# Optimization experiments

Hardware: AMD Instinct MI355X
Metric: run time of the kernel (lower is better)

The kernel has to match this reference:

```python
import jax, jax.numpy as jnp
import numpy as np

K, N = 4, 128
NODEDIM = 256
EDGEDIM_IN = 256
EDGEDIM_OUT = 256
GLOBALDIM = 256
INFODIM = 2 * NODEDIM + GLOBALDIM + EDGEDIM_IN  # 1024


def setup_inputs() -> dict:
    key = jax.random.key(0)
    ks = jax.random.split(key, 10)
    u = jax.random.normal(ks[0], (K, GLOBALDIM), dtype=jnp.float32)
    h_v = jax.random.normal(ks[1], (K, N, NODEDIM), dtype=jnp.float32)
    h_e = jax.random.normal(ks[2], (K, N, N, EDGEDIM_IN), dtype=jnp.float32)
    V = jax.random.randint(ks[3], (K, N), 0, 2).astype(jnp.float32)  # binary node mask
    E = jax.random.randint(ks[4], (K, N, N, 2), 0, 2, dtype=jnp.int32)  # per-type edge mask
    # function[1] params (loop runs i in [1, num_functions) -> only i=1)
    s1 = 1.0 / np.sqrt(INFODIM)
    W1 = jax.random.uniform(ks[5], (INFODIM, INFODIM), jnp.float32, -s1, s1)
    b1 = jax.random.uniform(ks[6], (INFODIM,), jnp.float32, -s1, s1)
    W2 = jax.random.uniform(ks[7], (INFODIM, EDGEDIM_OUT), jnp.float32, -s1, s1)
    b2 = jax.random.uniform(ks[8], (EDGEDIM_OUT,), jnp.float32, -s1, s1)
    return {"u": u, "h_v": h_v, "h_e": h_e, "V": V, "E": E,
            "W1": W1, "b1": b1, "W2": W2, "b2": b2}


def reference(u, h_v, h_e, V, E, W1, b1, W2, b2):
    Kb, Nn = h_v.shape[0], h_v.shape[1]
    hv = h_v * V[..., None]                                    # masked node states
    src = jnp.broadcast_to(hv[:, :, None, :], (Kb, Nn, Nn, NODEDIM))
    tgt = jnp.broadcast_to(hv[:, None, :, :], (Kb, Nn, Nn, NODEDIM))
    glb = jnp.broadcast_to(u[:, None, None, :], (Kb, Nn, Nn, GLOBALDIM))
    edge_feat = jnp.concatenate([src, tgt, glb, h_e], axis=-1)  # [K,N,N,INFODIM]
    # per-type MLP (only function index 1 executes for num_functions=2)
    h = jax.nn.elu(jnp.einsum('knmi,ij->knmj', edge_feat, W1) + b1)
    out = jnp.einsum('knmi,io->knmo', h, W2) + b2               # [K,N,N,EDGEDIM_OUT]
    mask = (E[..., 1] == 1)[..., None]
    h_e_update = jnp.where(mask, out, jnp.zeros((), out.dtype))
    # residual=True, history=True
    return h_e_update + h_e
```

## Files before the change

kernel.cpp:

```cpp
#include <hip/hip_runtime.h>
#include <stdint.h>

#define DEVI __device__ __forceinline__

typedef short bf16x8 __attribute__((ext_vector_type(8)));
typedef float f32x4  __attribute__((ext_vector_type(4)));

DEVI short f2bf(float f){
  union { float f; uint32_t u; } un; un.f = f;
  uint32_t u = un.u;
  u += 0x7fffu + ((u >> 16) & 1u);
  return (short)(u >> 16);
}
DEVI float bf2f(uint32_t us){
  union { uint32_t u; float f; } x; x.u = us << 16; return x.f;
}

DEVI f32x4 mfma16(bf16x8 a, bf16x8 b, f32x4 c){
  return __builtin_amdgcn_mfma_f32_16x16x32_bf16(a, b, c, 0, 0, 0);
}

__global__ void transpose_bf(const float* __restrict__ W, short* __restrict__ WT,
                             int R, int C){
  __shared__ float tile[32][33];
  int ctiles = C >> 5;
  int bi = blockIdx.x / ctiles, bj = blockIdx.x % ctiles;
  int tx = threadIdx.x & 31, ty = threadIdx.x >> 5;
  #pragma unroll
  for (int r = 0; r < 4; ++r){
    int i = bi*32 + ty + r*8;
    tile[ty + r*8][tx] = W[(size_t)i*C + bj*32 + tx];
  }
  __syncthreads();
  #pragma unroll
  for (int r = 0; r < 4; ++r){
    int j = bj*32 + ty + r*8;
    WT[(size_t)j*R + bi*32 + tx] = f2bf(tile[tx][ty + r*8]);
  }
}

__global__ void prep_hv(const float* __restrict__ hv, const float* __restrict__ V,
                        const float* __restrict__ u, short* __restrict__ hvb,
                        short* __restrict__ ub){
  int idx = blockIdx.x*256 + threadIdx.x;
  if (idx < 512*256){
    int r = idx >> 8;
    hvb[idx] = f2bf(hv[idx] * V[r]);
  } else if (idx < 512*256 + 1024){
    int i2 = idx - 512*256;
    ub[i2] = f2bf(u[i2]);
  }
}

__global__ __launch_bounds__(256) void prep_st(
    const short* __restrict__ hvb, const short* __restrict__ ub,
    const short* __restrict__ w1t, const float* __restrict__ b1,
    short* __restrict__ sbuf, short* __restrict__ tbuf)
{
  const int bid = blockIdx.x;
  const int st = bid >> 7;
  const int rt8 = (bid >> 4) & 7;
  const int ctile = bid & 15;
  const int r0 = rt8 << 6, j0 = ctile << 6;
  const int tid = threadIdx.x;
  const int w = tid >> 6, l = tid & 63;
  const int l15 = l & 15, l4 = l >> 4;
  __shared__ short A[64*256];
  __shared__ short Stile[64][64];
  for (int q = 0; q < 8; ++q){
    int id = tid + (q << 8);
    int row = id >> 5, c8 = id & 31;
    bf16x8 v = *(const bf16x8*)(hvb + (size_t)(r0 + row)*256 + c8*8);
    *(bf16x8*)((char*)A + row*512 + ((c8*16) ^ ((row & 7) << 4))) = v;
  }
  __syncthreads();
  const int wr = w >> 1, wc = w & 1;
  const int rowbase = wr << 5, colbase = wc << 5;
  const int swzA = (l15 & 7) << 4;
  f32x4 acc[2][2];
  acc[0][0]=0; acc[0][1]=0; acc[1][0]=0; acc[1][1]=0;
  const int ioff = st ? 256 : 0;
  const short* w1p = w1t + (size_t)(j0 + colbase + l15)*1024 + ioff + l4*8;
  const char* ap0 = (const char*)A + (rowbase + l15)*512;
  const char* ap1 = ap0 + 16*512;
  #pragma unroll
  for (int kk = 0; kk < 8; ++kk){
    int ib = kk*64 + l4*16;
    bf16x8 a0 = *(const bf16x8*)(ap0 + (ib ^ swzA));
    bf16x8 a1 = *(const bf16x8*)(ap1 + (ib ^ swzA));
    bf16x8 b0 = *(const bf16x8*)(w1p + kk*32);
    bf16x8 b1v = *(const bf16x8*)(w1p + 16*1024 + kk*32);
    acc[0][0] = mfma16(a0, b0, acc[0][0]);
    acc[1][0] = mfma16(a1, b0, acc[1][0]);
    acc[0][1] = mfma16(a0, b1v, acc[0][1]);
    acc[1][1] = mfma16(a1, b1v, acc[1][1]);
  }
  if (st == 0){
    const int kb = r0 >> 7;
    const short* up = ub + kb*256 + l4*8;
    const short* w1pu = w1t + (size_t)(j0 + colbase + l15)*1024 + 512 + l4*8;
    #pragma unroll
    for (int kk = 0; kk < 8; ++kk){
      bf16x8 au = *(const bf16x8*)(up + kk*32);
      bf16x8 b0 = *(const bf16x8*)(w1pu + kk*32);
      bf16x8 b1v = *(const bf16x8*)(w1pu + 16*1024 + kk*32);
      acc[0][0] = mfma16(au, b0, acc[0][0]);
      acc[1][0] = mfma16(au, b0, acc[1][0]);
      acc[0][1] = mfma16(au, b1v, acc[0][1]);
      acc[1][1] = mfma16(au, b1v, acc[1][1]);
    }
  }
  #pragma unroll
  for (int r = 0; r < 2; ++r){
    #pragma unroll
    for (int c = 0; c < 2; ++c){
      int jl = colbase + c*16 + l15;
      float badd = st ? 0.f : b1[j0 + jl];
      #pragma unroll
      for (int reg = 0; reg < 4; ++reg){
        int rowl = rowbase + r*16 + l4*4 + reg;
        short v = f2bf(acc[r][c][reg] + badd);
        if (st == 0) Stile[rowl][jl] = v;
        else         Stile[jl][rowl] = v;
      }
    }
  }
  __syncthreads();
  {
    int a = tid >> 2, ch = (tid & 3) << 4;
    bf16x8 v0 = *(const bf16x8*)(&Stile[a][ch]);
    bf16x8 v1 = *(const bf16x8*)(&Stile[a][ch + 8]);
    short* dst = (st == 0)
      ? (sbuf + (size_t)(r0 + a)*1024 + j0 + ch)
      : (tbuf + (size_t)(j0 + a)*512  + r0 + ch);
    *(bf16x8*)(dst)     = v0;
    *(bf16x8*)(dst + 8) = v1;
  }
}

__global__ __launch_bounds__(512, 2) void fused_edge(
    const float* __restrict__ he, const unsigned short* __restrict__ sb,
    const unsigned short* __restrict__ tbT, const short* __restrict__ w1t,
    const short* __restrict__ w2t, const float* __restrict__ b2,
    const int* __restrict__ Em, float* __restrict__ out)
{
  const int bo = blockIdx.x;
  const int b = ((bo & 7) << 6) | (bo >> 3);
  const int kp = b >> 8;
  const int n  = (b >> 1) & 127;
  const int m0 = (b & 1) << 6;
  const int k0 = kp << 1;
  const int tid = threadIdx.x;
  const int w = tid >> 6, l = tid & 63;
  const int l15 = l & 15, l4 = l >> 4;

  __shared__ short heb[128*256];
  __shared__ short eluv[2][128*128];
  __shared__ int   emask[128];

  const int base0 = (k0*128 + n)*128 + m0;

  #pragma unroll
  for (int q = 0; q < 8; ++q){
    int id = tid + (q << 9);
    int row = id >> 5, c8 = id & 31;
    size_t grow = (size_t)base0 + (row >> 6)*16384 + (row & 63);
    const float4* p = (const float4*)(he + grow*256 + c8*8);
    float4 a4 = p[0], b4 = p[1];
    union { bf16x8 v; short s[8]; } pk;
    pk.s[0]=f2bf(a4.x); pk.s[1]=f2bf(a4.y); pk.s[2]=f2bf(a4.z); pk.s[3]=f2bf(a4.w);
    pk.s[4]=f2bf(b4.x); pk.s[5]=f2bf(b4.y); pk.s[6]=f2bf(b4.z); pk.s[7]=f2bf(b4.w);
    *(bf16x8*)((char*)heb + row*512 + ((c8*16) ^ ((row & 7) << 4))) = pk.v;
  }
  if (tid < 128)
    emask[tid] = Em[((size_t)base0 + (tid >> 6)*16384 + (tid & 63))*2 + 1];
  __syncthreads();

  f32x4 acc2[8][2];
  #pragma unroll
  for (int i = 0; i < 8; ++i){ acc2[i][0] = 0; acc2[i][1] = 0; }

  const unsigned short* srow0 = sb + (size_t)(k0*128 + n)*1024;
  const unsigned short* srow1 = srow0 + 128*1024;
  const int tcol0 = k0*128 + m0;
  const int tcol1 = tcol0 + 128;
  const char* hb = (const char*)heb;
  const int swz = (l15 & 7) << 4;

  union u4 { ushort4 v; unsigned short s[4]; };

  bf16x8 bw1[8];
  {
    const short* w1p = w1t + (size_t)(w*16 + l15)*1024 + 768 + l4*8;
    #pragma unroll
    for (int kk = 0; kk < 8; ++kk) bw1[kk] = *(const bf16x8*)(w1p + kk*32);
  }
  u4 t4[8];
  #pragma unroll
  for (int rt = 0; rt < 8; ++rt){
    int tc = (rt < 4) ? (tcol0 + rt*16) : (tcol1 + (rt - 4)*16);
    t4[rt].v = *(const ushort4*)(tbT + (size_t)(w*16 + l15)*512 + tc + l4*4);
  }
  float sv0 = bf2f(srow0[w*16 + l15]);
  float sv1 = bf2f(srow1[w*16 + l15]);

  for (int ph = 0; ph < 8; ++ph){
    const int jcol = ph*128 + w*16 + l15;

    f32x4 acc1[8];
    #pragma unroll
    for (int i = 0; i < 8; ++i) acc1[i] = 0;
    #pragma unroll
    for (int kk = 0; kk < 8; ++kk){
      int ib = kk*64 + l4*16;
      #pragma unroll
      for (int rt = 0; rt < 8; ++rt){
        int row = rt*16 + l15;
        bf16x8 a = *(const bf16x8*)(hb + row*512 + (ib ^ swz));
        acc1[rt] = mfma16(a, bw1[kk], acc1[rt]);
      }
    }

    const short* w2p = w2t + (size_t)(w*32 + l15)*1024 + ph*128 + l4*8;
    bf16x8 bw2[2][4];
    #pragma unroll
    for (int ct = 0; ct < 2; ++ct)
      #pragma unroll
      for (int kk = 0; kk < 4; ++kk)
        bw2[ct][kk] = *(const bf16x8*)(w2p + (size_t)ct*16*1024 + kk*32);

    if (ph < 7){
      const short* w1p = w1t + (size_t)(jcol + 128)*1024 + 768 + l4*8;
      #pragma unroll
      for (int kk = 0; kk < 8; ++kk) bw1[kk] = *(const bf16x8*)(w1p + kk*32);
    }

    char* eb = (char*)(&eluv[ph & 1][0]);
    const int cb = (w*16 + l15)*2;
    #pragma unroll
    for (int rt = 0; rt < 8; ++rt){
      float sv = (rt < 4) ? sv0 : sv1;
      #pragma unroll
      for (int reg = 0; reg < 4; ++reg){
        int row = rt*16 + l4*4 + reg;
        float v = acc1[rt][reg] + sv + bf2f(t4[rt].s[reg]);
        v = v > 0.f ? v : (__expf(v) - 1.f);
        *(short*)(eb + row*256 + (cb ^ ((row & 7) << 4))) = f2bf(v);
      }
    }

    if (ph < 7){
      #pragma unroll
      for (int rt = 0; rt < 8; ++rt){
        int tc = (rt < 4) ? (tcol0 + rt*16) : (tcol1 + (rt - 4)*16);
        t4[rt].v = *(const ushort4*)(tbT + (size_t)(jcol + 128)*512 + tc + l4*4);
      }
      sv0 = bf2f(srow0[jcol + 128]);
      sv1 = bf2f(srow1[jcol + 128]);
    }
    __syncthreads();

    #pragma unroll
    for (int kk = 0; kk < 4; ++kk){
      int jb = kk*64 + l4*16;
      #pragma unroll
      for (int rt = 0; rt < 8; ++rt){
        int row = rt*16 + l15;
        bf16x8 a2 = *(const bf16x8*)(eb + row*256 + (jb ^ swz));
        acc2[rt][0] = mfma16(a2, bw2[0][kk], acc2[rt][0]);
        acc2[rt][1] = mfma16(a2, bw2[1][kk], acc2[rt][1]);
      }
    }
  }

  const float bias0 = b2[w*32 + l15];
  const float bias1 = b2[w*32 + 16 + l15];
  #pragma unroll
  for (int rt = 0; rt < 8; ++rt){
    #pragma unroll
    for (int reg = 0; reg < 4; ++reg){
      int row = rt*16 + l4*4 + reg;
      int e = emask[row];
      size_t grow = (size_t)base0 + (row >> 6)*16384 + (row & 63);
      float* op = out + grow*256 + w*32 + l15;
      const char* hrow = hb + row*512;
      int sw = (row & 7) << 4;
      float hv0 = bf2f(*(const unsigned short*)(hrow + (((w*32 + l15)*2) ^ sw)));
      float hv1 = bf2f(*(const unsigned short*)(hrow + (((w*32 + 16 + l15)*2) ^ sw)));
      op[0]  = ((e == 1) ? (acc2[rt][0][reg] + bias0) : 0.f) + hv0;
      op[16] = ((e == 1) ? (acc2[rt][1][reg] + bias1) : 0.f) + hv1;
    }
  }
}

extern "C" void kernel_launch(void* const* d_in, const int* in_sizes, int n_in,
                              void* d_out, int out_size, void* d_ws, size_t ws_size,
                              hipStream_t stream)
{
  const float* u   = (const float*)d_in[0];
  const float* h_v = (const float*)d_in[1];
  const float* h_e = (const float*)d_in[2];
  const float* V   = (const float*)d_in[3];
  const int*   E   = (const int*)d_in[4];
  const float* W1  = (const float*)d_in[5];
  const float* b1  = (const float*)d_in[6];
  const float* W2  = (const float*)d_in[7];
  const float* b2  = (const float*)d_in[8];
  float* out = (float*)d_out;

  char* ws = (char*)d_ws;
  short* w1t  = (short*)(ws);
  short* w2t  = (short*)(ws + (2u<<20));
  short* hvb  = (short*)(ws + (2u<<20) + (512u<<10));
  short* ub   = (short*)(ws + (2u<<20) + (768u<<10));
  short* sbuf = (short*)(ws + (3u<<20));
  short* tbuf = (short*)(ws + (4u<<20));

  transpose_bf<<<1024, 256, 0, stream>>>(W1, w1t, 1024, 1024);
  transpose_bf<<<256,  256, 0, stream>>>(W2, w2t, 1024, 256);
  prep_hv<<<516, 256, 0, stream>>>(h_v, V, u, hvb, ub);
  prep_st<<<256, 256, 0, stream>>>(hvb, ub, w1t, b1, sbuf, tbuf);
  fused_edge<<<512, 512, 0, stream>>>(h_e,
                                      (const unsigned short*)sbuf,
                                      (const unsigned short*)tbuf,
                                      w1t, w2t, b2, E, out);
}
```

Before: 181.7 us.

## Stage epilogue through LDS, change ELU swizzle, hoist prefetch, add setprio

```diff
diff --git a/kernel.cpp b/kernel.cpp
--- a/kernel.cpp
+++ b/kernel.cpp
@@ -210,6 +210,7 @@
     f32x4 acc1[8];
     #pragma unroll
     for (int i = 0; i < 8; ++i) acc1[i] = 0;
+    __builtin_amdgcn_s_setprio(1);
     #pragma unroll
     for (int kk = 0; kk < 8; ++kk){
       int ib = kk*64 + l4*16;
@@ -220,6 +221,7 @@
         acc1[rt] = mfma16(a, bw1[kk], acc1[rt]);
       }
     }
+    __builtin_amdgcn_s_setprio(0);
 
     const short* w2p = w2t + (size_t)(w*32 + l15)*1024 + ph*128 + l4*8;
     bf16x8 bw2[2][4];
@@ -229,10 +231,19 @@
       for (int kk = 0; kk < 4; ++kk)
         bw2[ct][kk] = *(const bf16x8*)(w2p + (size_t)ct*16*1024 + kk*32);
 
+    u4 t4n[8];
+    float sv0n = 0.f, sv1n = 0.f;
     if (ph < 7){
       const short* w1p = w1t + (size_t)(jcol + 128)*1024 + 768 + l4*8;
       #pragma unroll
       for (int kk = 0; kk < 8; ++kk) bw1[kk] = *(const bf16x8*)(w1p + kk*32);
+      #pragma unroll
+      for (int rt = 0; rt < 8; ++rt){
+        int tc = (rt < 4) ? (tcol0 + rt*16) : (tcol1 + (rt - 4)*16);
+        t4n[rt].v = *(const ushort4*)(tbT + (size_t)(jcol + 128)*512 + tc + l4*4);
+      }
+      sv0n = bf2f(srow0[jcol + 128]);
+      sv1n = bf2f(srow1[jcol + 128]);
     }
 
     char* eb = (char*)(&eluv[ph & 1][0]);
@@ -245,51 +256,65 @@
         int row = rt*16 + l4*4 + reg;
         float v = acc1[rt][reg] + sv + bf2f(t4[rt].s[reg]);
         v = v > 0.f ? v : (__expf(v) - 1.f);
-        *(short*)(eb + row*256 + (cb ^ ((row & 7) << 4))) = f2bf(v);
+        *(short*)(eb + row*256 + (cb ^ (((row >> 2) & 3) << 5))) = f2bf(v);
       }
     }
 
     if (ph < 7){
       #pragma unroll
-      for (int rt = 0; rt < 8; ++rt){
-        int tc = (rt < 4) ? (tcol0 + rt*16) : (tcol1 + (rt - 4)*16);
-        t4[rt].v = *(const ushort4*)(tbT + (size_t)(jcol + 128)*512 + tc + l4*4);
-      }
-      sv0 = bf2f(srow0[jcol + 128]);
-      sv1 = bf2f(srow1[jcol + 128]);
+      for (int rt = 0; rt < 8; ++rt) t4[rt] = t4n[rt];
+      sv0 = sv0n; sv1 = sv1n;
     }
     __syncthreads();
 
+    __builtin_amdgcn_s_setprio(1);
     #pragma unroll
     for (int kk = 0; kk < 4; ++kk){
       int jb = kk*64 + l4*16;
       #pragma unroll
       for (int rt = 0; rt < 8; ++rt){
         int row = rt*16 + l15;
-        bf16x8 a2 = *(const bf16x8*)(eb + row*256 + (jb ^ swz));
+        bf16x8 a2 = *(const bf16x8*)(eb + row*256 + (jb ^ (((row >> 2) & 3) << 5)));
         acc2[rt][0] = mfma16(a2, bw2[0][kk], acc2[rt][0]);
         acc2[rt][1] = mfma16(a2, bw2[1][kk], acc2[rt][1]);
       }
     }
-  }
-
+    __builtin_amdgcn_s_setprio(0);
+  }
+
+  __syncthreads();
   const float bias0 = b2[w*32 + l15];
   const float bias1 = b2[w*32 + 16 + l15];
-  #pragma unroll
-  for (int rt = 0; rt < 8; ++rt){
-    #pragma unroll
-    for (int reg = 0; reg < 4; ++reg){
-      int row = rt*16 + l4*4 + reg;
-      int e = emask[row];
+  float* stage = (float*)&eluv[0][0];
+  #pragma unroll
+  for (int c = 0; c < 4; ++c){
+    #pragma unroll
+    for (int rr = 0; rr < 2; ++rr){
+      int rt = c*2 + rr;
+      #pragma unroll
+      for (int reg = 0; reg < 4; ++reg){
+        int row = rt*16 + l4*4 + reg;
+        int srow = row & 31;
+        int e = emask[row];
+        const char* hrow = hb + row*512;
+        int sw = (row & 7) << 4;
+        float hv0 = bf2f(*(const unsigned short*)(hrow + (((w*32 + l15)*2) ^ sw)));
+        float hv1 = bf2f(*(const unsigned short*)(hrow + (((w*32 + 16 + l15)*2) ^ sw)));
+        stage[srow*260 + w*32 + l15]      = ((e == 1) ? (acc2[rt][0][reg] + bias0) : 0.f) + hv0;
+        stage[srow*260 + w*32 + 16 + l15] = ((e == 1) ? (acc2[rt][1][reg] + bias1) : 0.f) + hv1;
+      }
+    }
+    __syncthreads();
+    #pragma unroll
+    for (int p = 0; p < 4; ++p){
+      int id = tid + (p << 9);
+      int r32 = id >> 6, c4 = (id & 63) << 2;
+      f32x4 v = *(const f32x4*)(stage + r32*260 + c4);
+      int row = c*32 + r32;
       size_t grow = (size_t)base0 + (row >> 6)*16384 + (row & 63);
-      float* op = out + grow*256 + w*32 + l15;
-      const char* hrow = hb + row*512;
-      int sw = (row & 7) << 4;
-      float hv0 = bf2f(*(const unsigned short*)(hrow + (((w*32 + l15)*2) ^ sw)));
-      float hv1 = bf2f(*(const unsigned short*)(hrow + (((w*32 + 16 + l15)*2) ^ sw)));
-      op[0]  = ((e == 1) ? (acc2[rt][0][reg] + bias0) : 0.f) + hv0;
-      op[16] = ((e == 1) ? (acc2[rt][1][reg] + bias1) : 0.f) + hv1;
-    }
+      *(f32x4*)(out + grow*256 + c4) = v;
+    }
+    __syncthreads();
   }
 }
 
```

New measurement: 201.9 us. +11.1%, slower.
